# Performance work log

Hardware: AMD Instinct MI355X
Metric: run time of the kernel (lower is better)

Reference implementation:

```python
import jax, jax.numpy as jnp
import numpy as np

B, L, IN, H, W = 4096, 10, 8, 512, 512


def setup_inputs() -> dict:
    key = jax.random.key(0)
    ks = jax.random.split(key, 24)
    s = 0.05  # small init so tanh/sigmoid stay in active range
    def rn(k, shape):
        return jax.random.normal(k, shape, dtype=jnp.float32) * s
    return {
        "items": jax.random.normal(ks[0], (B, L, IN), dtype=jnp.float32),
        "decoder_items_input": jax.random.uniform(ks[1], (B, H), dtype=jnp.float32),
        "emb_w": rn(ks[2], (H, IN)), "emb_b": rn(ks[3], (H,)),
        "enc_wih": rn(ks[4], (3 * H, H)), "enc_whh": rn(ks[5], (3 * H, H)),
        "enc_bih": rn(ks[6], (3 * H,)), "enc_bhh": rn(ks[7], (3 * H,)),
        "dec_wih": rn(ks[8], (3 * H, H)), "dec_whh": rn(ks[9], (3 * H, H)),
        "dec_bih": rn(ks[10], (3 * H,)), "dec_bhh": rn(ks[11], (3 * H,)),
        "w1": rn(ks[12], (W, H)), "w2": rn(ks[13], (W, H)),
        "w3": rn(ks[14], (W, H)), "w4": rn(ks[15], (W, H)),
        "w5": rn(ks[16], (W, H)), "w6": rn(ks[17], (W, H)),
        "w7": rn(ks[18], (W, 2 * H)),
        "v1": rn(ks[19], (W,)), "v2": rn(ks[20], (W,)),
        "v3_w": rn(ks[21], (W,)), "v3_b": rn(ks[22], (1,)),
        "wori": rn(ks[23], (6, 3 * H)), "bori": jnp.zeros((6,), jnp.float32),
    }


def _gru_scan(xg, whh, bhh, h0):
    # xg: [L,B,3H] precomputed input-gate projections; returns all hidden states [L,B,H]
    def step(h, xg_t):
        hg = h @ whh.T + bhh
        xr, xz, xn = jnp.split(xg_t, 3, axis=-1)
        hr, hz, hn = jnp.split(hg, 3, axis=-1)
        r = jax.nn.sigmoid(xr + hr)
        z = jax.nn.sigmoid(xz + hz)
        n = jnp.tanh(xn + r * hn)
        h_new = (1.0 - z) * n + z * h
        return h_new, h_new
    _, ys = jax.lax.scan(step, h0, xg)
    return ys


def _forward(items, decoder_items_input, emb_w, emb_b, enc_wih, enc_whh, enc_bih, enc_bhh,
             dec_wih, dec_whh, dec_bih, dec_bhh, w1, w2, w3, w4, w5, w6, w7,
             v1, v2, v3_w, v3_b, wori, bori):
    Bsz, Lln, _ = items.shape
    Hh = emb_w.shape[0]
    x = items @ emb_w.T + emb_b                                  # [B,L,H] embedding
    xg = (x @ enc_wih.T + enc_bih).transpose(1, 0, 2)            # [L,B,3H]
    enc_out = _gru_scan(xg, enc_whh, enc_bhh, jnp.zeros((Bsz, Hh), x.dtype))  # [L,B,H]
    h0 = enc_out[-1]                                             # last encoder state
    enc_blh = enc_out.transpose(1, 0, 2)                         # [B,L,H]
    enc_w3 = enc_out @ w3.T                                      # [L,B,W] (hoisted, step-invariant)
    enc_w6 = enc_out @ w6.T                                      # [L,B,W]
    xg_dec = decoder_items_input @ dec_wih.T + dec_bih           # [B,3H] constant decoder input
    xr, xz, xn = jnp.split(xg_dec, 3, axis=-1)

    def step(h, _):
        hg = h @ dec_whh.T + dec_bhh
        hr, hz, hn = jnp.split(hg, 3, axis=-1)
        r = jax.nn.sigmoid(xr + hr)
        z = jax.nn.sigmoid(xz + hz)
        n = jnp.tanh(xn + r * hn)
        h_new = (1.0 - z) * n + z * h                            # GRUCell update
        # intra attention cache is always length-1 in the source (the shape[1]==1 branch
        # always fires), so log_softmax is over a singleton axis -> exactly zero.
        doi = h_new[:, None, :]                                  # [B,1,H]
        oi = jnp.tanh(h_new @ w1.T + h_new @ w2.T) @ v1          # [B]
        attnd = jax.nn.log_softmax(oi[:, None, None], axis=-1)   # [B,1,1] zeros
        hi = (attnd * doi).sum(axis=1)                           # [B,H] (zeros, faithful)
        sm = jnp.tanh(enc_w3 + h_new @ w4.T + hi @ w5.T)         # [L,B,W]
        out_seq = (sm @ v2).T                                    # [B,L]
        sm_ori = jnp.tanh(enc_w6 + jnp.concatenate([h_new, hi], axis=-1) @ w7.T)  # [L,B,W]
        oo = sm_ori @ v3_w + v3_b[0]                             # [L,B]
        attnc = jax.nn.log_softmax(oo.T[:, :, None], axis=-1)    # [B,L,1] zeros (singleton axis)
        he = (attnc * enc_blh).sum(axis=1)                       # [B,H]
        total = jnp.concatenate([he, h_new, hi], axis=-1)        # [B,3H]
        out_ori = total @ wori.T + bori                          # [B,6]
        return h_new, (out_seq, out_ori)

    _, (seqs, oris) = jax.lax.scan(step, h0, None, length=Lln)
    probs_seq = seqs.transpose(1, 0, 2)                          # [B,L,L]
    probs_ori = oris.transpose(1, 0, 2)                          # [B,L,6]
    return probs_seq, probs_ori


def reference(items, decoder_items_input, emb_w, emb_b, enc_wih, enc_whh, enc_bih, enc_bhh,
              dec_wih, dec_whh, dec_bih, dec_bhh, w1, w2, w3, w4, w5, w6, w7,
              v1, v2, v3_w, v3_b, wori, bori):
    return _forward(items, decoder_items_input, emb_w, emb_b, enc_wih, enc_whh, enc_bih,
                    enc_bhh, dec_wih, dec_whh, dec_bih, dec_bhh, w1, w2, w3, w4, w5, w6,
                    w7, v1, v2, v3_w, v3_b, wori, bori)
```

## Files before the change

kernel.cpp:

```cpp
#include <hip/hip_runtime.h>
#include <hip/hip_bf16.h>


#define B_   4096
#define L_   10
#define IN_  8
#define H_   512
#define H3_  1536
#define W_   512
#define ORI_BASE (B_ * L_ * L_)

typedef __attribute__((ext_vector_type(8))) short s8v;
typedef __attribute__((ext_vector_type(4))) short s4v;
typedef __attribute__((ext_vector_type(4))) float f4v;

#define LOG2E  1.4426950408889634f
#define LOG2E2 2.8853900817779268f

__device__ __forceinline__ float sig_fast(float x) {
  float e = __builtin_amdgcn_exp2f(-x * LOG2E);
  return __builtin_amdgcn_rcpf(1.f + e);
}
__device__ __forceinline__ float tanh_fast(float x) {
  float e = __builtin_amdgcn_exp2f(x * LOG2E2);
  return 1.f - 2.f * __builtin_amdgcn_rcpf(e + 1.f);
}
__device__ __forceinline__ short f2bf(float f) {
  __hip_bfloat16 h = __float2bfloat16(f);
  return __builtin_bit_cast(short, h);
}
__device__ __forceinline__ float bf2f(short s) {
  __hip_bfloat16 h = __builtin_bit_cast(__hip_bfloat16, s);
  return __bfloat162float(h);
}
__device__ __forceinline__ void stc(float* p, float v) { *p = v; }
__device__ __forceinline__ void stc(short* p, float v) { *p = f2bf(v); }

__global__ __launch_bounds__(256) void prep_all(
    const float* __restrict__ s0, short* __restrict__ d0,
    const float* __restrict__ s1, short* __restrict__ d1,
    const float* __restrict__ s2, short* __restrict__ d2,
    const float* __restrict__ s3, short* __restrict__ d3,
    const float* __restrict__ s4, short* __restrict__ d4,
    const float* __restrict__ s5, short* __restrict__ d5)
{
  long i8 = (long)blockIdx.x * 256 + threadIdx.x;
  const float* s; short* d; long off;
  if      (i8 < 98304)  { s = s0; d = d0; off = i8; }
  else if (i8 < 196608) { s = s1; d = d1; off = i8 - 98304; }
  else if (i8 < 294912) { s = s2; d = d2; off = i8 - 196608; }
  else if (i8 < 327680) { s = s3; d = d3; off = i8 - 294912; }
  else if (i8 < 360448) { s = s4; d = d4; off = i8 - 327680; }
  else if (i8 < 622592) { s = s5; d = d5; off = i8 - 360448; }
  else return;
  const float* sp = s + off * 8;
  s8v v;
#pragma unroll
  for (int j = 0; j < 8; ++j) v[j] = f2bf(sp[j]);
  *(s8v*)(d + off * 8) = v;
}

__global__ __launch_bounds__(256) void build_wc(
    const float* __restrict__ enc_wih, const float* __restrict__ emb_w,
    const float* __restrict__ emb_b, const float* __restrict__ enc_bih,
    float* __restrict__ Wc, float* __restrict__ bc)
{
  __shared__ float se[H_ * IN_];
  __shared__ float sb[H_];
  const int tid = threadIdx.x;
  for (int i = tid; i < H_ * IN_; i += 256) se[i] = emb_w[i];
  for (int i = tid; i < H_; i += 256) sb[i] = emb_b[i];
  __syncthreads();
  int g = (blockIdx.x * 256 + tid) >> 6;
  int lane = tid & 63;
  const float* wr = enc_wih + (long)g * H_ + lane * 8;
  float w8[8];
#pragma unroll
  for (int j = 0; j < 8; ++j) w8[j] = wr[j];
  float acc[9] = {};
#pragma unroll
  for (int kk = 0; kk < 8; ++kk) {
    int k = lane * 8 + kk;
#pragma unroll
    for (int j = 0; j < 8; ++j) acc[j] += w8[kk] * se[k * IN_ + j];
    acc[8] += w8[kk] * sb[k];
  }
#pragma unroll
  for (int j = 0; j < 9; ++j)
#pragma unroll
    for (int off = 32; off; off >>= 1) acc[j] += __shfl_down(acc[j], off, 64);
  if (lane == 0) {
#pragma unroll
    for (int j = 0; j < 8; ++j) Wc[g * IN_ + j] = acc[j];
    bc[g] = acc[8] + enc_bih[g];
  }
}

template <typename CT>
__global__ __launch_bounds__(256) void gemm_bf16(
    const short* __restrict__ A, long lda,
    const short* __restrict__ Bw, long ldb,
    const float* __restrict__ bias,
    CT* __restrict__ C, long ldc, int K, float scale)
{
  __shared__ short As[2][128 * 64];
  __shared__ short Bs[2][128 * 64];
  const int tid = threadIdx.x;
  const long row0 = (long)blockIdx.y * 128;
  const long col0 = (long)blockIdx.x * 128;
  const int wave = tid >> 6, lane = tid & 63;
  const int wm = (wave & 1) * 64, wn = (wave >> 1) * 64;
  const int r16 = lane & 15, quad = lane >> 4;
  const int sw = r16 & 7;
  f4v acc[4][4] = {};

  auto stage = [&](int buf, int k0) {
#pragma unroll
    for (int r = 0; r < 4; ++r) {
      int idx = r * 256 + tid;
      int m = idx >> 3, c8 = idx & 7;
      int src = c8 ^ (m & 7);
      __builtin_amdgcn_global_load_lds(
          (const __attribute__((address_space(1))) void*)(A + (row0 + m) * lda + k0 + src * 8),
          (__attribute__((address_space(3))) void*)(&As[buf][idx * 8]), 16, 0, 0);
    }
#pragma unroll
    for (int r = 0; r < 4; ++r) {
      int idx = r * 256 + tid;
      int m = idx >> 3, c8 = idx & 7;
      int src = c8 ^ (m & 7);
      __builtin_amdgcn_global_load_lds(
          (const __attribute__((address_space(1))) void*)(Bw + (col0 + m) * ldb + k0 + src * 8),
          (__attribute__((address_space(3))) void*)(&Bs[buf][idx * 8]), 16, 0, 0);
    }
  };

  const int nk = K >> 6;
  stage(0, 0);
  for (int k = 0; k < nk; ++k) {
    if (k < nk - 1) {
      stage((k + 1) & 1, (k + 1) * 64);
      asm volatile("s_waitcnt vmcnt(8)" ::: "memory");
    } else {
      asm volatile("s_waitcnt vmcnt(0)" ::: "memory");
    }
    __builtin_amdgcn_s_barrier();
    const short* Asc = As[k & 1];
    const short* Bsc = Bs[k & 1];
    s8v af[4][2], bf[4][2];
#pragma unroll
    for (int i = 0; i < 4; ++i)
#pragma unroll
      for (int hh = 0; hh < 2; ++hh)
        af[i][hh] = *(const s8v*)&Asc[(wm + i * 16 + r16) * 64 + ((hh * 4 + quad) ^ sw) * 8];
#pragma unroll
    for (int j = 0; j < 4; ++j)
#pragma unroll
      for (int hh = 0; hh < 2; ++hh)
        bf[j][hh] = *(const s8v*)&Bsc[(wn + j * 16 + r16) * 64 + ((hh * 4 + quad) ^ sw) * 8];
    __builtin_amdgcn_s_setprio(1);
#pragma unroll
    for (int hh = 0; hh < 2; ++hh)
#pragma unroll
      for (int i = 0; i < 4; ++i)
#pragma unroll
        for (int j = 0; j < 4; ++j)
          acc[i][j] = __builtin_amdgcn_mfma_f32_16x16x32_bf16(af[i][hh], bf[j][hh], acc[i][j], 0, 0, 0);
    __builtin_amdgcn_s_setprio(0);
    __builtin_amdgcn_s_barrier();
  }

#pragma unroll
  for (int i = 0; i < 4; ++i) {
    long rbase = row0 + wm + i * 16 + quad * 4;
#pragma unroll
    for (int j = 0; j < 4; ++j) {
      long c = col0 + wn + j * 16 + r16;
      float bv = bias ? bias[c] : 0.f;
#pragma unroll
      for (int rg = 0; rg < 4; ++rg)
        stc(&C[(rbase + rg) * ldc + c], (acc[i][j][rg] + bv) * scale);
    }
  }
}

__global__ __launch_bounds__(256) void gemm_epi(
    const short* __restrict__ Ae, const short* __restrict__ Ad,
    const short* __restrict__ w3b, const short* __restrict__ w4b,
    short* __restrict__ Ce, short* __restrict__ Cd)
{
  const short* A  = blockIdx.z ? Ad : Ae;
  const short* Bw = blockIdx.z ? w4b : w3b;
  short* C        = blockIdx.z ? Cd : Ce;
  __shared__ short As[2][128 * 64];
  __shared__ short Bs[2][128 * 64];
  const int tid = threadIdx.x;
  const long row0 = (long)blockIdx.y * 128;
  const long col0 = (long)blockIdx.x * 128;
  const int wave = tid >> 6, lane = tid & 63;
  const int wm = (wave & 1) * 64, wn = (wave >> 1) * 64;
  const int r16 = lane & 15, quad = lane >> 4;
  const int sw = r16 & 7;
  f4v acc[4][4] = {};

  auto stage = [&](int buf, int k0) {
#pragma unroll
    for (int r = 0; r < 4; ++r) {
      int idx = r * 256 + tid;
      int m = idx >> 3, c8 = idx & 7;
      int src = c8 ^ (m & 7);
      __builtin_amdgcn_global_load_lds(
          (const __attribute__((address_space(1))) void*)(A + (row0 + m) * H_ + k0 + src * 8),
          (__attribute__((address_space(3))) void*)(&As[buf][idx * 8]), 16, 0, 0);
    }
#pragma unroll
    for (int r = 0; r < 4; ++r) {
      int idx = r * 256 + tid;
      int m = idx >> 3, c8 = idx & 7;
      int src = c8 ^ (m & 7);
      __builtin_amdgcn_global_load_lds(
          (const __attribute__((address_space(1))) void*)(Bw + (col0 + m) * H_ + k0 + src * 8),
          (__attribute__((address_space(3))) void*)(&Bs[buf][idx * 8]), 16, 0, 0);
    }
  };

  stage(0, 0);
  for (int k = 0; k < 8; ++k) {
    if (k < 7) {
      stage((k + 1) & 1, (k + 1) * 64);
      asm volatile("s_waitcnt vmcnt(8)" ::: "memory");
    } else {
      asm volatile("s_waitcnt vmcnt(0)" ::: "memory");
    }
    __builtin_amdgcn_s_barrier();
    const short* Asc = As[k & 1];
    const short* Bsc = Bs[k & 1];
    s8v af[4][2], bf[4][2];
#pragma unroll
    for (int i = 0; i < 4; ++i)
#pragma unroll
      for (int hh = 0; hh < 2; ++hh)
        af[i][hh] = *(const s8v*)&Asc[(wm + i * 16 + r16) * 64 + ((hh * 4 + quad) ^ sw) * 8];
#pragma unroll
    for (int j = 0; j < 4; ++j)
#pragma unroll
      for (int hh = 0; hh < 2; ++hh)
        bf[j][hh] = *(const s8v*)&Bsc[(wn + j * 16 + r16) * 64 + ((hh * 4 + quad) ^ sw) * 8];
    __builtin_amdgcn_s_setprio(1);
#pragma unroll
    for (int hh = 0; hh < 2; ++hh)
#pragma unroll
      for (int i = 0; i < 4; ++i)
#pragma unroll
        for (int j = 0; j < 4; ++j)
          acc[i][j] = __builtin_amdgcn_mfma_f32_16x16x32_bf16(af[i][hh], bf[j][hh], acc[i][j], 0, 0, 0);
    __builtin_amdgcn_s_setprio(0);
    __builtin_amdgcn_s_barrier();
  }

#pragma unroll
  for (int i = 0; i < 4; ++i) {
    long rbase = row0 + wm + i * 16 + quad * 4;
#pragma unroll
    for (int j = 0; j < 4; ++j) {
      long c = col0 + wn + j * 16 + r16;
#pragma unroll
      for (int rg = 0; rg < 4; ++rg)
        C[(rbase + rg) * W_ + c] = f2bf(acc[i][j][rg] * LOG2E2);
    }
  }
}

template <bool ENC>
__global__ __launch_bounds__(256) void gru_fused(
    const short* __restrict__ Aprev,
    const short* __restrict__ Whh,
    const float* __restrict__ bhh,
    const short* __restrict__ xg,
    const float* __restrict__ items_t,
    const float* __restrict__ Wc,
    const float* __restrict__ bc,
    short* __restrict__ hout)
{
  __shared__ short As[2][64 * 64];
  __shared__ short Bs[2][192 * 64];
  const int tid = threadIdx.x;
  const int flat = blockIdx.x;
  const int by = flat & 63, bx = flat >> 6;
  const long row0 = (long)by * 64;
  const int col0 = bx * 64;
  const int wave = tid >> 6, lane = tid & 63;
  const int r16 = lane & 15, quad = lane >> 4;
  const int sw = r16 & 7;

  f4v acc[3][4] = {};

  auto stage = [&](int buf, int k0) {
#pragma unroll
    for (int r = 0; r < 2; ++r) {
      int idx = r * 256 + tid;
      int m = idx >> 3, c8 = idx & 7;
      int src = c8 ^ (m & 7);
      __builtin_amdgcn_global_load_lds(
          (const __attribute__((address_space(1))) void*)(Aprev + (row0 + m) * H_ + k0 + src * 8),
          (__attribute__((address_space(3))) void*)(&As[buf][idx * 8]), 16, 0, 0);
    }
#pragma unroll
    for (int r = 0; r < 6; ++r) {
      int idx = r * 256 + tid;
      int m = idx >> 3, c8 = idx & 7;
      int src = c8 ^ (m & 7);
      int g = m >> 6, cc = m & 63;
      __builtin_amdgcn_global_load_lds(
          (const __attribute__((address_space(1))) void*)(Whh + ((long)g * H_ + col0 + cc) * H_ + k0 + src * 8),
          (__attribute__((address_space(3))) void*)(&Bs[buf][idx * 8]), 16, 0, 0);
    }
  };

  stage(0, 0);
  int cur = 0;
  for (int k = 0; k < 8; ++k) {
    if (k < 7) {
      stage(cur ^ 1, (k + 1) * 64);
      asm volatile("s_waitcnt vmcnt(8)" ::: "memory");
    } else {
      asm volatile("s_waitcnt vmcnt(0)" ::: "memory");
    }
    __builtin_amdgcn_s_barrier();
    s8v af[4][2], bf[3][2];
#pragma unroll
    for (int i = 0; i < 4; ++i)
#pragma unroll
      for (int hh = 0; hh < 2; ++hh)
        af[i][hh] = *(const s8v*)&As[cur][(i * 16 + r16) * 64 + ((hh * 4 + quad) ^ sw) * 8];
#pragma unroll
    for (int g = 0; g < 3; ++g)
#pragma unroll
      for (int hh = 0; hh < 2; ++hh)
        bf[g][hh] = *(const s8v*)&Bs[cur][(g * 64 + wave * 16 + r16) * 64 + ((hh * 4 + quad) ^ sw) * 8];
    __builtin_amdgcn_s_setprio(1);
#pragma unroll
    for (int hh = 0; hh < 2; ++hh)
#pragma unroll
      for (int g = 0; g < 3; ++g)
#pragma unroll
        for (int i = 0; i < 4; ++i)
          acc[g][i] = __builtin_amdgcn_mfma_f32_16x16x32_bf16(af[i][hh], bf[g][hh], acc[g][i], 0, 0, 0);
    __builtin_amdgcn_s_setprio(0);
    __builtin_amdgcn_s_barrier();
    cur ^= 1;
  }

  const int col = col0 + wave * 16 + r16;
  float wc[3][8], bcv[3];
  if (ENC) {
#pragma unroll
    for (int g = 0; g < 3; ++g) {
      const float* wr = Wc + ((long)g * H_ + col) * IN_;
#pragma unroll
      for (int j = 0; j < 8; ++j) wc[g][j] = wr[j];
      bcv[g] = bc[g * H_ + col];
    }
    float* itemS = (float*)As;
    int i2 = tid * 2;
    int m = i2 >> 3, j = i2 & 7;
    itemS[i2] = items_t[(row0 + m) * (L_ * IN_) + j];
    itemS[i2 + 1] = items_t[(row0 + m) * (L_ * IN_) + j + 1];
    __syncthreads();
  }
  float bhr = bhh[col], bhz = bhh[col + H_], bhn = bhh[col + 2 * H_];

#pragma unroll
  for (int i = 0; i < 4; ++i) {
#pragma unroll
    for (int rg = 0; rg < 4; ++rg) {
      int rl = i * 16 + quad * 4 + rg;
      long row = row0 + rl;
      float xr, xz, xn;
      if (ENC) {
        const float* it = (const float*)As + rl * 8;
        xr = bcv[0]; xz = bcv[1]; xn = bcv[2];
#pragma unroll
        for (int j = 0; j < 8; ++j) {
          float iv = it[j];
          xr += iv * wc[0][j];
          xz += iv * wc[1][j];
          xn += iv * wc[2][j];
        }
      } else {
        long gx = row * H3_ + col;
        xr = bf2f(xg[gx]); xz = bf2f(xg[gx + H_]); xn = bf2f(xg[gx + 2 * H_]);
      }
      float r = sig_fast(xr + acc[0][i][rg] + bhr);
      float z = sig_fast(xz + acc[1][i][rg] + bhz);
      float n = tanh_fast(xn + r * (acc[2][i][rg] + bhn));
      long hi = row * H_ + col;
      float hp = bf2f(Aprev[hi]);
      float hv = (1.f - z) * n + z * hp;
      hout[hi] = f2bf(hv);
    }
  }
}

__global__ __launch_bounds__(256) void out_seq_all(
    const short* __restrict__ ew3,
    const short* __restrict__ a4,
    const float* __restrict__ v2,
    float* __restrict__ out)
{
  __shared__ short s_e[L_ * W_];
  __shared__ short s_a[L_ * W_];
  __shared__ short v2b[W_];
  __shared__ float part[7 * 4 * 4 * 4];
  __shared__ float svtot_s;
  const int b = blockIdx.x;
  const int tid = threadIdx.x;
  const int w = tid >> 6, lane = tid & 63;
  const int r16 = lane & 15, quad = lane >> 4;

  for (int i = tid; i < L_ * 64; i += 256) {
    int row = i >> 6, c = i & 63;
    int swc = (c ^ (row & 7)) * 8;
    *(s8v*)(s_e + row * W_ + swc) = *(const s8v*)(ew3 + ((long)row * B_ + b) * W_ + c * 8);
    *(s8v*)(s_a + row * W_ + swc) = *(const s8v*)(a4  + ((long)row * B_ + b) * W_ + c * 8);
  }
  {
    int i = tid * 2;
    v2b[i] = f2bf(v2[i]);
    v2b[i + 1] = f2bf(v2[i + 1]);
  }
  if (w == 0) {
    float s = 0.f;
    const float* vp = v2 + lane * 8;
#pragma unroll
    for (int j = 0; j < 8; ++j) s += vp[j];
#pragma unroll
    for (int off = 32; off; off >>= 1) s += __shfl_down(s, off, 64);
    if (lane == 0) svtot_s = s;
  }
  __syncthreads();

  s8v vfrag[4];
#pragma unroll
  for (int j = 0; j < 4; ++j)
    vfrag[j] = *(const s8v*)(v2b + (w * 4 + j) * 32 + quad * 8);

  f4v acc[7] = {};
#pragma unroll
  for (int g = 0; g < 7; ++g) {
    int p = g * 16 + r16;
    int t = (p * 205) >> 11;
    int l = p - t * 10;
    if (t > 9) t = 9;
    const short* ep = s_e + l * W_;
    const short* ap = s_a + t * W_;
    const int le = l & 7, ta = t & 7;
#pragma unroll
    for (int j = 0; j < 4; ++j) {
      int cb = (w * 4 + j) * 4 + quad;
      s8v ev = *(const s8v*)(ep + (cb ^ le) * 8);
      s8v av = *(const s8v*)(ap + (cb ^ ta) * 8);
      s8v sf;
#pragma unroll
      for (int e = 0; e < 8; ++e) {
        float x = bf2f(ev[e]) + bf2f(av[e]);
        float s = __builtin_amdgcn_rcpf(__builtin_amdgcn_exp2f(x) + 1.f);
        sf[e] = f2bf(s);
      }
      acc[g] = __builtin_amdgcn_mfma_f32_16x16x32_bf16(sf, vfrag[j], acc[g], 0, 0, 0);
    }
  }

  if (r16 == 0) {
#pragma unroll
    for (int g = 0; g < 7; ++g)
      *(f4v*)(part + ((g * 4 + quad) * 4 + w) * 4) = acc[g];
  }
  __syncthreads();
  if (tid < 112) {
    int g = tid >> 4, row = tid & 15;
    int q = row >> 2, rg = row & 3;
    float s = 0.f;
#pragma unroll
    for (int ww = 0; ww < 4; ++ww)
      s += part[((g * 4 + q) * 4 + ww) * 4 + rg];
    int p = g * 16 + row;
    if (p < 100) {
      int t = (p * 205) >> 11;
      int l = p - t * 10;
      out[((long)b * L_ + t) * L_ + l] = svtot_s - 2.f * s;
    }
  }
}

__global__ __launch_bounds__(256) void out_ori_all(
    const short* __restrict__ dh,
    const float* __restrict__ wori, const float* __restrict__ bori,
    float* __restrict__ out)
{
  int wid = (blockIdx.x * 256 + threadIdx.x) >> 6;
  int lane = threadIdx.x & 63;
  int b = wid / L_, t = wid - b * L_;
  s8v hv = *(const s8v*)(dh + ((long)t * B_ + b) * H_ + lane * 8);
  float hf[8];
#pragma unroll
  for (int j = 0; j < 8; ++j) hf[j] = bf2f(hv[j]);
  float res[6];
#pragma unroll
  for (int o = 0; o < 6; ++o) {
    const float* wr = wori + (long)o * H3_ + H_ + lane * 8;
    float acc = 0.f;
#pragma unroll
    for (int j = 0; j < 8; ++j) acc += hf[j] * wr[j];
#pragma unroll
    for (int off = 32; off; off >>= 1) acc += __shfl_down(acc, off, 64);
    res[o] = acc;
  }
  if (lane == 0) {
    float* po = out + ORI_BASE + ((long)b * L_ + t) * 6;
#pragma unroll
    for (int o = 0; o < 6; ++o) po[o] = res[o] + bori[o];
  }
}

extern "C" void kernel_launch(void* const* d_in, const int* in_sizes, int n_in,
                              void* d_out, int out_size, void* d_ws, size_t ws_size,
                              hipStream_t stream)
{
  const float* items   = (const float*)d_in[0];
  const float* dec_in  = (const float*)d_in[1];
  const float* emb_w   = (const float*)d_in[2];
  const float* emb_b   = (const float*)d_in[3];
  const float* enc_wih = (const float*)d_in[4];
  const float* enc_whh = (const float*)d_in[5];
  const float* enc_bih = (const float*)d_in[6];
  const float* enc_bhh = (const float*)d_in[7];
  const float* dec_wih = (const float*)d_in[8];
  const float* dec_whh = (const float*)d_in[9];
  const float* dec_bih = (const float*)d_in[10];
  const float* dec_bhh = (const float*)d_in[11];
  const float* w3      = (const float*)d_in[14];
  const float* w4      = (const float*)d_in[15];
  const float* v2      = (const float*)d_in[20];
  const float* wori    = (const float*)d_in[23];
  const float* bori    = (const float*)d_in[24];
  float* out = (float*)d_out;

  char* ws = (char*)d_ws;
  size_t off = 0;
  auto alloc = [&](size_t bytes) { size_t o = off; off += (bytes + 255) & ~255UL; return o; };
  float* Wc       = (float*)(ws + alloc(H3_ * IN_ * 4));
  float* bc       = (float*)(ws + alloc(H3_ * 4));
  short* xgb      = (short*)(ws + alloc((size_t)B_ * H3_ * 2));
  short* enc_hist = (short*)(ws + alloc((size_t)11 * B_ * H_ * 2));
  short* dec_hist = (short*)(ws + alloc((size_t)L_ * B_ * H_ * 2));
  short* ew3      = (short*)(ws + alloc((size_t)L_ * B_ * W_ * 2));
  short* a4       = (short*)(ws + alloc((size_t)L_ * B_ * W_ * 2));
  short* whh_e    = (short*)(ws + alloc((size_t)H3_ * H_ * 2));
  short* whh_d    = (short*)(ws + alloc((size_t)H3_ * H_ * 2));
  short* wih_d    = (short*)(ws + alloc((size_t)H3_ * H_ * 2));
  short* w3b      = (short*)(ws + alloc((size_t)W_ * H_ * 2));
  short* w4b      = (short*)(ws + alloc((size_t)W_ * H_ * 2));
  short* decb     = (short*)(ws + alloc((size_t)B_ * H_ * 2));

  prep_all<<<(622592 + 255) / 256, 256, 0, stream>>>(
      enc_whh, whh_e, dec_whh, whh_d, dec_wih, wih_d,
      w3, w3b, w4, w4b, dec_in, decb);
  build_wc<<<384, 256, 0, stream>>>(enc_wih, emb_w, emb_b, enc_bih, Wc, bc);

  hipMemsetAsync(enc_hist, 0, (size_t)B_ * H_ * 2, stream);

  gemm_bf16<short><<<dim3(12, 32), 256, 0, stream>>>(
      decb, H_, wih_d, H_, dec_bih, xgb, H3_, H_, 1.f);

  for (int t = 0; t < L_; ++t) {
    gru_fused<true><<<512, 256, 0, stream>>>(
        enc_hist + (size_t)t * B_ * H_, whh_e, enc_bhh, nullptr,
        items + (size_t)t * IN_, Wc, bc,
        enc_hist + (size_t)(t + 1) * B_ * H_);
  }

  for (int t = 0; t < L_; ++t) {
    const short* prev = (t == 0) ? enc_hist + (size_t)10 * B_ * H_
                                 : dec_hist + (size_t)(t - 1) * B_ * H_;
    gru_fused<false><<<512, 256, 0, stream>>>(
        prev, whh_d, dec_bhh, xgb, nullptr, nullptr, nullptr,
        dec_hist + (size_t)t * B_ * H_);
  }

  gemm_epi<<<dim3(4, 320, 2), 256, 0, stream>>>(
      enc_hist + (size_t)B_ * H_, dec_hist, w3b, w4b, ew3, a4);
  out_seq_all<<<B_, 256, 0, stream>>>(ew3, a4, v2, out);
  out_ori_all<<<(B_ * L_) / 4, 256, 0, stream>>>(dec_hist, wori, bori, out);
}
```

Baseline: 530.8 us.

## Pre-permute GRU recurrent weights into MFMA fragment order and load B directly to registers

```diff
diff --git a/kernel.cpp b/kernel.cpp
--- a/kernel.cpp
+++ b/kernel.cpp
@@ -37,8 +37,6 @@
 __device__ __forceinline__ void stc(short* p, float v) { *p = f2bf(v); }
 
 __global__ __launch_bounds__(256) void prep_all(
-    const float* __restrict__ s0, short* __restrict__ d0,
-    const float* __restrict__ s1, short* __restrict__ d1,
     const float* __restrict__ s2, short* __restrict__ d2,
     const float* __restrict__ s3, short* __restrict__ d3,
     const float* __restrict__ s4, short* __restrict__ d4,
@@ -46,18 +44,36 @@
 {
   long i8 = (long)blockIdx.x * 256 + threadIdx.x;
   const float* s; short* d; long off;
-  if      (i8 < 98304)  { s = s0; d = d0; off = i8; }
-  else if (i8 < 196608) { s = s1; d = d1; off = i8 - 98304; }
-  else if (i8 < 294912) { s = s2; d = d2; off = i8 - 196608; }
-  else if (i8 < 327680) { s = s3; d = d3; off = i8 - 294912; }
-  else if (i8 < 360448) { s = s4; d = d4; off = i8 - 327680; }
-  else if (i8 < 622592) { s = s5; d = d5; off = i8 - 360448; }
+  if      (i8 < 98304)  { s = s2; d = d2; off = i8; }
+  else if (i8 < 131072) { s = s3; d = d3; off = i8 - 98304; }
+  else if (i8 < 163840) { s = s4; d = d4; off = i8 - 131072; }
+  else if (i8 < 425984) { s = s5; d = d5; off = i8 - 163840; }
   else return;
   const float* sp = s + off * 8;
   s8v v;
 #pragma unroll
   for (int j = 0; j < 8; ++j) v[j] = f2bf(sp[j]);
   *(s8v*)(d + off * 8) = v;
+}
+
+__global__ __launch_bounds__(256) void prep_w2(
+    const float* __restrict__ enc_whh, const float* __restrict__ dec_whh,
+    short* __restrict__ W2e, short* __restrict__ W2d)
+{
+  int tg = blockIdx.x * 256 + threadIdx.x;
+  const float* src = enc_whh; short* dst = W2e;
+  int t = tg;
+  if (t >= 98304) { t -= 98304; src = dec_whh; dst = W2d; }
+  int l = t & 63;
+  int u = t >> 6;
+  int hh = u & 1, kb = (u >> 1) & 7, c16 = (u >> 4) & 31, g = u >> 9;
+  int row = g * 512 + c16 * 16 + (l & 15);
+  int colb = kb * 64 + hh * 32 + (l >> 4) * 8;
+  const float* sp = src + (long)row * 512 + colb;
+  s8v v;
+#pragma unroll
+  for (int j = 0; j < 8; ++j) v[j] = f2bf(sp[j]);
+  *(s8v*)(dst + (long)t * 8) = v;
 }
 
 __global__ __launch_bounds__(256) void build_wc(
@@ -274,7 +290,7 @@
 template <bool ENC>
 __global__ __launch_bounds__(256) void gru_fused(
     const short* __restrict__ Aprev,
-    const short* __restrict__ Whh,
+    const short* __restrict__ W2,
     const float* __restrict__ bhh,
     const short* __restrict__ xg,
     const float* __restrict__ items_t,
@@ -283,7 +299,6 @@
     short* __restrict__ hout)
 {
   __shared__ short As[2][64 * 64];
-  __shared__ short Bs[2][192 * 64];
   const int tid = threadIdx.x;
   const int flat = blockIdx.x;
   const int by = flat & 63, bx = flat >> 6;
@@ -292,10 +307,13 @@
   const int wave = tid >> 6, lane = tid & 63;
   const int r16 = lane & 15, quad = lane >> 4;
   const int sw = r16 & 7;
+  const int c16 = bx * 4 + wave;
+  const int col = col0 + wave * 16 + r16;
 
   f4v acc[3][4] = {};
-
-  auto stage = [&](int buf, int k0) {
+  s8v bfr[2][3][2];
+
+  auto stageA = [&](int buf, int k0) {
 #pragma unroll
     for (int r = 0; r < 2; ++r) {
       int idx = r * 256 + tid;
@@ -305,39 +323,33 @@
           (const __attribute__((address_space(1))) void*)(Aprev + (row0 + m) * H_ + k0 + src * 8),
           (__attribute__((address_space(3))) void*)(&As[buf][idx * 8]), 16, 0, 0);
     }
-#pragma unroll
-    for (int r = 0; r < 6; ++r) {
-      int idx = r * 256 + tid;
-      int m = idx >> 3, c8 = idx & 7;
-      int src = c8 ^ (m & 7);
-      int g = m >> 6, cc = m & 63;
-      __builtin_amdgcn_global_load_lds(
-          (const __attribute__((address_space(1))) void*)(Whh + ((long)g * H_ + col0 + cc) * H_ + k0 + src * 8),
-          (__attribute__((address_space(3))) void*)(&Bs[buf][idx * 8]), 16, 0, 0);
-    }
   };
-
-  stage(0, 0);
+  auto loadB = [&](s8v (&dst)[3][2], int kb) {
+#pragma unroll
+    for (int g = 0; g < 3; ++g)
+#pragma unroll
+      for (int hh = 0; hh < 2; ++hh)
+        dst[g][hh] = *(const s8v*)(W2 + ((((long)(g * 32 + c16) * 8 + kb) * 2 + hh) * 512) + lane * 8);
+  };
+
+  stageA(0, 0);
+  loadB(bfr[0], 0);
   int cur = 0;
   for (int k = 0; k < 8; ++k) {
     if (k < 7) {
-      stage(cur ^ 1, (k + 1) * 64);
+      stageA(cur ^ 1, (k + 1) * 64);
+      loadB(bfr[(k + 1) & 1], k + 1);
       asm volatile("s_waitcnt vmcnt(8)" ::: "memory");
     } else {
       asm volatile("s_waitcnt vmcnt(0)" ::: "memory");
     }
     __builtin_amdgcn_s_barrier();
-    s8v af[4][2], bf[3][2];
+    s8v af[4][2];
 #pragma unroll
     for (int i = 0; i < 4; ++i)
 #pragma unroll
       for (int hh = 0; hh < 2; ++hh)
         af[i][hh] = *(const s8v*)&As[cur][(i * 16 + r16) * 64 + ((hh * 4 + quad) ^ sw) * 8];
-#pragma unroll
-    for (int g = 0; g < 3; ++g)
-#pragma unroll
-      for (int hh = 0; hh < 2; ++hh)
-        bf[g][hh] = *(const s8v*)&Bs[cur][(g * 64 + wave * 16 + r16) * 64 + ((hh * 4 + quad) ^ sw) * 8];
     __builtin_amdgcn_s_setprio(1);
 #pragma unroll
     for (int hh = 0; hh < 2; ++hh)
@@ -345,13 +357,12 @@
       for (int g = 0; g < 3; ++g)
 #pragma unroll
         for (int i = 0; i < 4; ++i)
-          acc[g][i] = __builtin_amdgcn_mfma_f32_16x16x32_bf16(af[i][hh], bf[g][hh], acc[g][i], 0, 0, 0);
+          acc[g][i] = __builtin_amdgcn_mfma_f32_16x16x32_bf16(af[i][hh], bfr[k & 1][g][hh], acc[g][i], 0, 0, 0);
     __builtin_amdgcn_s_setprio(0);
     __builtin_amdgcn_s_barrier();
     cur ^= 1;
   }
 
-  const int col = col0 + wave * 16 + r16;
   float wc[3][8], bcv[3];
   if (ENC) {
 #pragma unroll
@@ -556,16 +567,16 @@
   short* dec_hist = (short*)(ws + alloc((size_t)L_ * B_ * H_ * 2));
   short* ew3      = (short*)(ws + alloc((size_t)L_ * B_ * W_ * 2));
   short* a4       = (short*)(ws + alloc((size_t)L_ * B_ * W_ * 2));
-  short* whh_e    = (short*)(ws + alloc((size_t)H3_ * H_ * 2));
-  short* whh_d    = (short*)(ws + alloc((size_t)H3_ * H_ * 2));
+  short* W2e      = (short*)(ws + alloc((size_t)H3_ * H_ * 2));
+  short* W2d      = (short*)(ws + alloc((size_t)H3_ * H_ * 2));
   short* wih_d    = (short*)(ws + alloc((size_t)H3_ * H_ * 2));
   short* w3b      = (short*)(ws + alloc((size_t)W_ * H_ * 2));
   short* w4b      = (short*)(ws + alloc((size_t)W_ * H_ * 2));
   short* decb     = (short*)(ws + alloc((size_t)B_ * H_ * 2));
 
-  prep_all<<<(622592 + 255) / 256, 256, 0, stream>>>(
-      enc_whh, whh_e, dec_whh, whh_d, dec_wih, wih_d,
-      w3, w3b, w4, w4b, dec_in, decb);
+  prep_all<<<(425984 + 255) / 256, 256, 0, stream>>>(
+      dec_wih, wih_d, w3, w3b, w4, w4b, dec_in, decb);
+  prep_w2<<<768, 256, 0, stream>>>(enc_whh, dec_whh, W2e, W2d);
   build_wc<<<384, 256, 0, stream>>>(enc_wih, emb_w, emb_b, enc_bih, Wc, bc);
 
   hipMemsetAsync(enc_hist, 0, (size_t)B_ * H_ * 2, stream);
@@ -575,7 +586,7 @@
 
   for (int t = 0; t < L_; ++t) {
     gru_fused<true><<<512, 256, 0, stream>>>(
-        enc_hist + (size_t)t * B_ * H_, whh_e, enc_bhh, nullptr,
+        enc_hist + (size_t)t * B_ * H_, W2e, enc_bhh, nullptr,
         items + (size_t)t * IN_, Wc, bc,
         enc_hist + (size_t)(t + 1) * B_ * H_);
   }
@@ -584,7 +595,7 @@
     const short* prev = (t == 0) ? enc_hist + (size_t)10 * B_ * H_
                                  : dec_hist + (size_t)(t - 1) * B_ * H_;
     gru_fused<false><<<512, 256, 0, stream>>>(
-        prev, whh_d, dec_bhh, xgb, nullptr, nullptr, nullptr,
+        prev, W2d, dec_bhh, xgb, nullptr, nullptr, nullptr,
         dec_hist + (size_t)t * B_ * H_);
   }
 
```

Measured after the change: 528.0 us. About the same (-0.5%).
